# Performance work log

Hardware: AMD Instinct MI355X
Metric: run time of the kernel (lower is better)

The kernel has to match this reference:

```python
import jax, jax.numpy as jnp
import numpy as np

DIM = 256
NUM_HEADS = 4
HEAD_DIM = DIM // NUM_HEADS


def setup_inputs() -> dict:
    key = jax.random.key(0)
    ks = jax.random.split(key, 8)
    B, N, C = 4, 2048, DIM
    x = jax.random.normal(ks[0], (B, N, C), dtype=jnp.float32)
    R = jax.random.normal(ks[1], (B, 3, 3), dtype=jnp.float32)
    P = jax.random.normal(ks[2], (N, 3), dtype=jnp.float32)
    s = 1.0 / np.sqrt(C)
    qkv_w = jax.random.normal(ks[3], (3 * C, C), dtype=jnp.float32) * s
    qkv_b = jax.random.normal(ks[4], (3 * C,), dtype=jnp.float32) * 0.02
    proj_w = jax.random.normal(ks[5], (C, C), dtype=jnp.float32) * s
    proj_b = jax.random.normal(ks[6], (C,), dtype=jnp.float32) * 0.02
    pos_scale = jnp.asarray(1.0, dtype=jnp.float32)
    return {"x": x, "R": R, "P": P, "qkv_w": qkv_w, "qkv_b": qkv_b,
            "proj_w": proj_w, "proj_b": proj_b, "pos_scale": pos_scale}


def reference(x, R, P, qkv_w, qkv_b, proj_w, proj_b, pos_scale):
    B, N, C = x.shape
    H, D = NUM_HEADS, HEAD_DIM
    scale = D ** -0.5
    # qkv: (B,N,3C) -> (3,B,H,N,D)
    qkv = (x @ qkv_w.T + qkv_b).reshape(B, N, 3, H, D).transpose(2, 0, 3, 1, 4)
    q, k, v = qkv[0], qkv[1], qkv[2]
    # attention logits (B,H,N,N)
    attn = jnp.einsum('bhid,bhjd->bhij', q, k) * scale
    # positional bias: RP = (R @ P^T)^T -> (B,N,3); bias_ij = dot(RP_i, P_j)
    RP = jnp.einsum('bab,jb->bja', R, P) if False else jnp.einsum('bca,ja->bjc', jnp.swapaxes(R, 1, 2), P)
    RP = jnp.einsum('bcd,jd->bjc', R, P)  # (B,N,3): (R @ P.T).T
    bias = jnp.einsum('bik,jk->bij', RP, P)[:, None, :, :] * pos_scale  # (B,1,N,N) broadcast over heads
    attn = jax.nn.softmax(attn + bias, axis=-1)
    out = jnp.einsum('bhij,bhjd->bhid', attn, v)  # (B,H,N,D)
    out = out.transpose(0, 2, 1, 3).reshape(B, N, C)
    out = out @ proj_w.T + proj_b
    return out
```

## Files before the change

kernel.cpp:

```cpp
#include <hip/hip_runtime.h>
#include <hip/hip_bf16.h>

#define B_ 4
#define N_ 2048
#define C_ 256
#define H_ 4
#define D_ 64

typedef __attribute__((ext_vector_type(8))) short bf16x8;
typedef __attribute__((ext_vector_type(4))) float f32x4;

#define LOG2E 1.4426950408889634f

static __device__ inline unsigned short f2bf(float f) {
    unsigned u = __builtin_bit_cast(unsigned, f);
    unsigned r = (u + 0x7fffu + ((u >> 16) & 1u)) >> 16;
    return (unsigned short)r;
}
static __device__ inline float bf2f(unsigned short h) {
    unsigned u = ((unsigned)h) << 16;
    return __builtin_bit_cast(float, u);
}
static __device__ inline unsigned pack2(float a, float b) {
    __hip_bfloat162 h = __float22bfloat162_rn(make_float2(a, b));
    unsigned u;
    __builtin_memcpy(&u, &h, 4);
    return u;
}
static __device__ inline bf16x8 ld_frag(const unsigned short* p) {
    return __builtin_bit_cast(bf16x8, *(const uint4*)p);
}

__global__ __launch_bounds__(256) void cvt_kernel(
    const float* __restrict__ x, const float* __restrict__ qkv_w,
    const float* __restrict__ proj_w,
    unsigned short* __restrict__ xb, unsigned short* __restrict__ wqb,
    unsigned short* __restrict__ wpb)
{
    const int bid = blockIdx.x, tid = threadIdx.x;
    const float* s; unsigned short* d; int i;
    if (bid < 1024)      { s = x;      d = xb;  i = (bid * 256 + tid) * 8; }
    else if (bid < 1120) { s = qkv_w;  d = wqb; i = ((bid - 1024) * 256 + tid) * 8; }
    else                 { s = proj_w; d = wpb; i = ((bid - 1120) * 256 + tid) * 8; }
    float4 a = *(const float4*)(s + i);
    float4 b = *(const float4*)(s + i + 4);
    uint4 u;
    u.x = pack2(a.x, a.y); u.y = pack2(a.z, a.w);
    u.z = pack2(b.x, b.y); u.w = pack2(b.z, b.w);
    *(uint4*)(d + i) = u;
}

__global__ __launch_bounds__(256) void qkv_gemm(
    const unsigned short* __restrict__ xb, const unsigned short* __restrict__ wb,
    const float* __restrict__ bias, unsigned short* __restrict__ qb,
    unsigned short* __restrict__ kb, unsigned short* __restrict__ vt)
{
    __shared__ __align__(16) unsigned short As[128 * 40];
    __shared__ __align__(16) unsigned short Bs[128 * 40];
    const int m0 = blockIdx.x * 128, o0 = blockIdx.y * 128;
    const int tid = threadIdx.x;
    const int wave = tid >> 6, lane = tid & 63, quad = lane >> 4, l16 = lane & 15;
    const int wy = wave >> 1, wx = wave & 1;

    f32x4 acc[4][4];
    #pragma unroll
    for (int i = 0; i < 4; ++i)
        #pragma unroll
        for (int j = 0; j < 4; ++j) acc[i][j] = (f32x4){0.f, 0.f, 0.f, 0.f};

    const int srow = tid >> 1, soff = (tid & 1) * 16;

    for (int k0 = 0; k0 < 256; k0 += 32) {
        __syncthreads();
        {
            const unsigned short* sa = &xb[(size_t)(m0 + srow) * 256 + k0 + soff];
            const unsigned short* sb = &wb[(size_t)(o0 + srow) * 256 + k0 + soff];
            *(uint4*)&As[srow * 40 + soff + 0] = *(const uint4*)(sa + 0);
            *(uint4*)&As[srow * 40 + soff + 8] = *(const uint4*)(sa + 8);
            *(uint4*)&Bs[srow * 40 + soff + 0] = *(const uint4*)(sb + 0);
            *(uint4*)&Bs[srow * 40 + soff + 8] = *(const uint4*)(sb + 8);
        }
        __syncthreads();
        bf16x8 a[4], b[4];
        #pragma unroll
        for (int mt = 0; mt < 4; ++mt) a[mt] = ld_frag(&As[(wy * 64 + mt * 16 + l16) * 40 + quad * 8]);
        #pragma unroll
        for (int nt = 0; nt < 4; ++nt) b[nt] = ld_frag(&Bs[(wx * 64 + nt * 16 + l16) * 40 + quad * 8]);
        #pragma unroll
        for (int mt = 0; mt < 4; ++mt)
            #pragma unroll
            for (int nt = 0; nt < 4; ++nt)
                acc[mt][nt] = __builtin_amdgcn_mfma_f32_16x16x32_bf16(a[mt], b[nt], acc[mt][nt], 0, 0, 0);
    }

    const int sec = o0 + wx * 64;
    const int three = sec >> 8;
    const int h = (sec >> 6) & 3;
    const int b = m0 >> 11;
    float bv[4];
    #pragma unroll
    for (int nt = 0; nt < 4; ++nt) bv[nt] = bias[sec + nt * 16 + l16];

    if (three == 2) {
        const int n64 = (m0 + wy * 64) & 2047;
        const size_t bh64 = ((size_t)b * H_ + h) * 64;
        #pragma unroll
        for (int nt = 0; nt < 4; ++nt) {
            int d = nt * 16 + l16;
            #pragma unroll
            for (int r = 0; r < 4; ++r) {
                ushort4 v;
                v.x = f2bf(acc[0][nt][r] + bv[nt]);
                v.y = f2bf(acc[1][nt][r] + bv[nt]);
                v.z = f2bf(acc[2][nt][r] + bv[nt]);
                v.w = f2bf(acc[3][nt][r] + bv[nt]);
                *(ushort4*)&vt[(bh64 + d) * N_ + n64 + 16 * quad + 4 * r] = v;
            }
        }
    } else {
        unsigned short* dst = (three == 0) ? qb : kb;
        float sc = (three == 0) ? (0.125f * LOG2E) : 1.0f;
        #pragma unroll
        for (int mt = 0; mt < 4; ++mt)
            #pragma unroll
            for (int r = 0; r < 4; ++r) {
                int n = (m0 + wy * 64 + mt * 16 + quad * 4 + r) & 2047;
                size_t rowbase = (((size_t)b * H_ + h) * N_ + n) * D_;
                #pragma unroll
                for (int nt = 0; nt < 4; ++nt)
                    dst[rowbase + nt * 16 + l16] = f2bf((acc[mt][nt][r] + bv[nt]) * sc);
            }
    }
}

#define LDK 72
#define LDKX 104

__global__ __launch_bounds__(256) void attn_kernel(
    const unsigned short* __restrict__ qb, const unsigned short* __restrict__ kb,
    const unsigned short* __restrict__ vt,
    const float* __restrict__ Rm, const float* __restrict__ Pm,
    const float* __restrict__ ps_ptr,
    unsigned short* __restrict__ Opart, float* __restrict__ ml)
{
    __shared__ __align__(16) unsigned short Ks[64 * LDKX];
    __shared__ __align__(16) unsigned short Vs[64 * LDK];
    __shared__ __align__(16) unsigned short Ps[64 * LDK];

    const int bh = blockIdx.y;
    const int b = bh >> 2;
    const int i0 = blockIdx.x * 64;
    const int split = blockIdx.z;
    const int tid = threadIdx.x;
    const int wave = tid >> 6, lane = tid & 63;
    const int quad = lane >> 4, l16 = lane & 15;
    const float ps = ps_ptr[0];

    const size_t base = (size_t)bh * N_ * D_;
    const unsigned short* qg = qb + base;
    const unsigned short* kg = kb + base;
    const unsigned short* vg = vt + base;

    if (tid < 64) {
        uint4 z = {0u, 0u, 0u, 0u};
        *(uint4*)&Ks[tid * LDKX + 80] = z;
        *(uint4*)&Ks[tid * LDKX + 88] = z;
    }

    const int qrow = i0 + wave * 16 + l16;
    bf16x8 aq[3];
    #pragma unroll
    for (int ks = 0; ks < 2; ++ks)
        aq[ks] = ld_frag(&qg[(size_t)qrow * D_ + ks * 32 + quad * 8]);

    {
        float p0 = Pm[qrow * 3 + 0], p1 = Pm[qrow * 3 + 1], p2 = Pm[qrow * 3 + 2];
        float sc = ps * LOG2E;
        unsigned short ah[3], al[3];
        #pragma unroll
        for (int c = 0; c < 3; ++c) {
            float a = (Rm[b * 9 + c * 3 + 0] * p0 + Rm[b * 9 + c * 3 + 1] * p1
                     + Rm[b * 9 + c * 3 + 2] * p2) * sc;
            ah[c] = f2bf(a);
            al[c] = f2bf(a - bf2f(ah[c]));
        }
        bf16x8 e = (bf16x8){0,0,0,0,0,0,0,0};
        if (quad == 0) {
            e[0] = (short)ah[0]; e[1] = (short)ah[1]; e[2] = (short)ah[2];
            e[3] = (short)ah[0]; e[4] = (short)ah[1]; e[5] = (short)ah[2];
            e[6] = (short)al[0]; e[7] = (short)al[1];
        } else if (quad == 1) {
            e[0] = (short)al[2];
        }
        aq[2] = e;
    }

    const bf16x8 ones = (bf16x8){0x3F80,0x3F80,0x3F80,0x3F80,0x3F80,0x3F80,0x3F80,0x3F80};

    float m_run = -1e30f;
    f32x4 o_acc[4], lacc;
    #pragma unroll
    for (int t = 0; t < 4; ++t) o_acc[t] = (f32x4){0.f, 0.f, 0.f, 0.f};
    lacc = (f32x4){0.f, 0.f, 0.f, 0.f};

    const int jbeg = split * (N_ / 2);
    const int NT = (N_ / 2) / 64;

    for (int jt = 0; jt < NT; ++jt) {
        const int j0 = jbeg + jt * 64;
        __syncthreads();
        #pragma unroll
        for (int rr = 0; rr < 2; ++rr) {
            int c = tid + rr * 256;
            int row = c >> 3, off = (c & 7) * 8;
            *(uint4*)&Ks[row * LDKX + off] = *(const uint4*)&kg[(size_t)(j0 + row) * D_ + off];
            *(uint4*)&Vs[row * LDK + off] = *(const uint4*)&vg[(size_t)row * N_ + j0 + off];
        }
        if (tid < 64) {
            const float* pp = &Pm[(size_t)(j0 + tid) * 3];
            float p0 = pp[0], p1 = pp[1], p2 = pp[2];
            unsigned u0 = f2bf(p0), u1 = f2bf(p1), u2 = f2bf(p2);
            unsigned v0 = f2bf(p0 - bf2f((unsigned short)u0));
            unsigned v1 = f2bf(p1 - bf2f((unsigned short)u1));
            unsigned v2 = f2bf(p2 - bf2f((unsigned short)u2));
            uint4 lo, hi;
            lo.x = u0 | (u1 << 16); lo.y = u2 | (v0 << 16);
            lo.z = v1 | (v2 << 16); lo.w = u0 | (u1 << 16);
            hi.x = u2; hi.y = 0u; hi.z = 0u; hi.w = 0u;
            *(uint4*)&Ks[tid * LDKX + 64] = lo;
            *(uint4*)&Ks[tid * LDKX + 72] = hi;
        }
        __syncthreads();

        f32x4 s[4];
        #pragma unroll
        for (int t = 0; t < 4; ++t) {
            f32x4 c = {0.f, 0.f, 0.f, 0.f};
            #pragma unroll
            for (int ks = 0; ks < 3; ++ks) {
                bf16x8 bk = ld_frag(&Ks[(l16 + 16 * t) * LDKX + ks * 32 + quad * 8]);
                c = __builtin_amdgcn_mfma_f32_16x16x32_bf16(aq[ks], bk, c, 0, 0, 0);
            }
            s[t] = c;
        }

        float mx = m_run;
        #pragma unroll
        for (int t = 0; t < 4; ++t)
            #pragma unroll
            for (int r = 0; r < 4; ++r)
                mx = fmaxf(mx, s[t][r]);
        #pragma unroll
        for (int off = 1; off < 64; off <<= 1)
            mx = fmaxf(mx, __shfl_xor(mx, off));
        const float alpha = exp2f(m_run - mx);
        m_run = mx;

        #pragma unroll
        for (int r = 0; r < 4; ++r) {
            float p0 = exp2f(s[0][r] - mx), p1 = exp2f(s[1][r] - mx);
            float p2 = exp2f(s[2][r] - mx), p3 = exp2f(s[3][r] - mx);
            uint2 w;
            w.x = pack2(p0, p1);
            w.y = pack2(p2, p3);
            *(uint2*)&Ps[(wave * 16 + quad * 4 + r) * LDK + 4 * l16] = w;
        }

        if (alpha < 1.0f) {
            #pragma unroll
            for (int t = 0; t < 4; ++t)
                #pragma unroll
                for (int r = 0; r < 4; ++r)
                    o_acc[t][r] *= alpha;
            #pragma unroll
            for (int r = 0; r < 4; ++r) lacc[r] *= alpha;
        }

        #pragma unroll
        for (int ks = 0; ks < 2; ++ks) {
            bf16x8 ap = ld_frag(&Ps[(wave * 16 + l16) * LDK + ks * 32 + quad * 8]);
            #pragma unroll
            for (int t = 0; t < 4; ++t) {
                bf16x8 bv = ld_frag(&Vs[(l16 + 16 * t) * LDK + ks * 32 + quad * 8]);
                o_acc[t] = __builtin_amdgcn_mfma_f32_16x16x32_bf16(ap, bv, o_acc[t], 0, 0, 0);
            }
            lacc = __builtin_amdgcn_mfma_f32_16x16x32_bf16(ap, ones, lacc, 0, 0, 0);
        }
    }

    const size_t pbase = (size_t)(split * 16 + bh) * N_;
    #pragma unroll
    for (int r = 0; r < 4; ++r) {
        int row = i0 + wave * 16 + quad * 4 + r;
        #pragma unroll
        for (int t = 0; t < 4; ++t)
            Opart[(pbase + row) * D_ + l16 + 16 * t] = f2bf(o_acc[t][r]);
        if (l16 == 0) {
            float2* mlp = (float2*)ml;
            mlp[pbase + row] = make_float2(m_run, lacc[r]);
        }
    }
}

__global__ __launch_bounds__(256) void proj_gemm(
    const unsigned short* __restrict__ Opart, const float* __restrict__ ml,
    const unsigned short* __restrict__ wb, const float* __restrict__ bias,
    float* __restrict__ out)
{
    __shared__ __align__(16) unsigned short As[64 * 40];
    __shared__ __align__(16) unsigned short Bs[64 * 40];
    const int m0 = blockIdx.x * 64, o0 = blockIdx.y * 64;
    const int tid = threadIdx.x;
    const int wave = tid >> 6, lane = tid & 63, quad = lane >> 4, l16 = lane & 15;
    const float2* mlp = (const float2*)ml;

    const int srow = tid >> 2, scb = (tid & 3) * 8;
    const int sm = m0 + srow, sb = sm >> 11, sn = sm & 2047;

    float w1h[4], w2h[4];
    #pragma unroll
    for (int h = 0; h < 4; ++h) {
        size_t r1 = (size_t)(sb * 4 + h) * N_ + sn;
        float2 ml1 = mlp[r1], ml2 = mlp[r1 + 16 * N_];
        float mm = fmaxf(ml1.x, ml2.x);
        float w1 = exp2f(ml1.x - mm), w2 = exp2f(ml2.x - mm);
        float inv = 1.f / (ml1.y * w1 + ml2.y * w2);
        w1h[h] = w1 * inv; w2h[h] = w2 * inv;
    }

    f32x4 acc[4];
    #pragma unroll
    for (int j = 0; j < 4; ++j) acc[j] = (f32x4){0.f, 0.f, 0.f, 0.f};

    for (int k0 = 0; k0 < 256; k0 += 32) {
        const int h = k0 >> 6;
        const int d0 = (k0 & 63) + scb;
        __syncthreads();
        {
            size_t r1 = (size_t)(sb * 4 + h) * N_ + sn;
            union { uint4 u; unsigned short s[8]; } a1, a2;
            a1.u = *(const uint4*)&Opart[r1 * D_ + d0];
            a2.u = *(const uint4*)&Opart[(r1 + 16 * N_) * D_ + d0];
            float w1 = w1h[h], w2 = w2h[h];
            uint4 mv;
            unsigned* mp = (unsigned*)&mv;
            #pragma unroll
            for (int j = 0; j < 4; ++j)
                mp[j] = pack2(bf2f(a1.s[2*j]) * w1 + bf2f(a2.s[2*j]) * w2,
                              bf2f(a1.s[2*j+1]) * w1 + bf2f(a2.s[2*j+1]) * w2);
            *(uint4*)&As[srow * 40 + scb] = mv;
            *(uint4*)&Bs[srow * 40 + scb] = *(const uint4*)&wb[(size_t)(o0 + srow) * 256 + k0 + scb];
        }
        __syncthreads();
        bf16x8 a = ld_frag(&As[(wave * 16 + l16) * 40 + quad * 8]);
        #pragma unroll
        for (int nt = 0; nt < 4; ++nt) {
            bf16x8 b = ld_frag(&Bs[(nt * 16 + l16) * 40 + quad * 8]);
            acc[nt] = __builtin_amdgcn_mfma_f32_16x16x32_bf16(a, b, acc[nt], 0, 0, 0);
        }
    }

    float bv[4];
    #pragma unroll
    for (int nt = 0; nt < 4; ++nt) bv[nt] = bias[o0 + nt * 16 + l16];
    #pragma unroll
    for (int r = 0; r < 4; ++r) {
        int m = m0 + wave * 16 + quad * 4 + r;
        #pragma unroll
        for (int nt = 0; nt < 4; ++nt)
            out[(size_t)m * 256 + o0 + nt * 16 + l16] = acc[nt][r] + bv[nt];
    }
}

extern "C" void kernel_launch(void* const* d_in, const int* in_sizes, int n_in,
                              void* d_out, int out_size, void* d_ws, size_t ws_size,
                              hipStream_t stream) {
    const float* x       = (const float*)d_in[0];
    const float* Rm      = (const float*)d_in[1];
    const float* Pm      = (const float*)d_in[2];
    const float* qkv_w   = (const float*)d_in[3];
    const float* qkv_b   = (const float*)d_in[4];
    const float* proj_w  = (const float*)d_in[5];
    const float* proj_b  = (const float*)d_in[6];
    const float* pos_scl = (const float*)d_in[7];
    float* out = (float*)d_out;

    const size_t NE = (size_t)B_ * H_ * N_ * D_;
    unsigned short* xb    = (unsigned short*)d_ws;
    unsigned short* wqb   = xb   + NE;
    unsigned short* wpb   = wqb  + 768 * 256;
    unsigned short* qb    = wpb  + 256 * 256;
    unsigned short* kb    = qb   + NE;
    unsigned short* vtb   = kb   + NE;
    unsigned short* opart = vtb  + NE;
    float*          mlb   = (float*)(opart + 2 * NE);

    cvt_kernel<<<1152, 256, 0, stream>>>(x, qkv_w, proj_w, xb, wqb, wpb);
    qkv_gemm<<<dim3(64, 6), 256, 0, stream>>>(xb, wqb, qkv_b, qb, kb, vtb);
    attn_kernel<<<dim3(32, 16, 2), 256, 0, stream>>>(qb, kb, vtb, Rm, Pm, pos_scl, opart, mlb);
    proj_gemm<<<dim3(128, 4), 256, 0, stream>>>(opart, mlb, wpb, proj_b, out);
}
```

Baseline: 140.1 us.

## Replace online softmax max with a precomputed Cauchy-Schwarz upper bound

Computes a per-row upper bound on the logits from the query norm times the max key norm plus the positional-vector norm times the max |P| norm, using a new norm_kernel and a reduction appended to cvt_kernel. The attention loop then exponentiates against this fixed bound instead of tracking a running max. This removes the per-tile max reduction, shuffles and rescaling of the accumulators, and lets the split-combine in the projection reduce to a plain sum. The cost is an extra small kernel and atomics, plus a risk of underflow when the bound is far above the true max, which can lose precision or make the row sum zero.

```diff
diff --git a/kernel.cpp b/kernel.cpp
--- a/kernel.cpp
+++ b/kernel.cpp
@@ -33,10 +33,11 @@
 
 __global__ __launch_bounds__(256) void cvt_kernel(
     const float* __restrict__ x, const float* __restrict__ qkv_w,
-    const float* __restrict__ proj_w,
+    const float* __restrict__ proj_w, const float* __restrict__ Pm,
     unsigned short* __restrict__ xb, unsigned short* __restrict__ wqb,
-    unsigned short* __restrict__ wpb)
+    unsigned short* __restrict__ wpb, unsigned* __restrict__ nb)
 {
+    __shared__ float red[256];
     const int bid = blockIdx.x, tid = threadIdx.x;
     const float* s; unsigned short* d; int i;
     if (bid < 1024)      { s = x;      d = xb;  i = (bid * 256 + tid) * 8; }
@@ -48,6 +49,24 @@
     u.x = pack2(a.x, a.y); u.y = pack2(a.z, a.w);
     u.z = pack2(b.x, b.y); u.w = pack2(b.z, b.w);
     *(uint4*)(d + i) = u;
+
+    if (bid == 1151) {
+        float mp = 0.f;
+        #pragma unroll
+        for (int r = 0; r < 8; ++r) {
+            int n = tid * 8 + r;
+            float p0 = Pm[n * 3 + 0], p1 = Pm[n * 3 + 1], p2 = Pm[n * 3 + 2];
+            mp = fmaxf(mp, p0 * p0 + p1 * p1 + p2 * p2);
+        }
+        red[tid] = mp;
+        __syncthreads();
+        for (int w = 128; w > 0; w >>= 1) {
+            if (tid < w) red[tid] = fmaxf(red[tid], red[tid + w]);
+            __syncthreads();
+        }
+        if (tid < 16) nb[tid] = 0u;
+        if (tid == 0) nb[16] = __builtin_bit_cast(unsigned, red[0]);
+    }
 }
 
 __global__ __launch_bounds__(256) void qkv_gemm(
@@ -133,6 +152,29 @@
     }
 }
 
+__global__ __launch_bounds__(256) void norm_kernel(
+    const unsigned short* __restrict__ kb, unsigned* __restrict__ nb)
+{
+    __shared__ float red[256];
+    const int bh = blockIdx.x, chunk = blockIdx.y, tid = threadIdx.x;
+    const size_t base = (size_t)bh * N_ * D_ + (size_t)(chunk * 256 + tid) * D_;
+    float sk = 0.f;
+    #pragma unroll
+    for (int j4 = 0; j4 < 8; ++j4) {
+        union { uint4 u; unsigned short s[8]; } kv;
+        kv.u = *(const uint4*)&kb[base + j4 * 8];
+        #pragma unroll
+        for (int j = 0; j < 8; ++j) { float v = bf2f(kv.s[j]); sk += v * v; }
+    }
+    red[tid] = sk;
+    __syncthreads();
+    for (int w = 128; w > 0; w >>= 1) {
+        if (tid < w) red[tid] = fmaxf(red[tid], red[tid + w]);
+        __syncthreads();
+    }
+    if (tid == 0) atomicMax(&nb[bh], __builtin_bit_cast(unsigned, red[0]));
+}
+
 #define LDK 72
 #define LDKX 104
 
@@ -140,7 +182,7 @@
     const unsigned short* __restrict__ qb, const unsigned short* __restrict__ kb,
     const unsigned short* __restrict__ vt,
     const float* __restrict__ Rm, const float* __restrict__ Pm,
-    const float* __restrict__ ps_ptr,
+    const float* __restrict__ ps_ptr, const unsigned* __restrict__ nb,
     unsigned short* __restrict__ Opart, float* __restrict__ ml)
 {
     __shared__ __align__(16) unsigned short Ks[64 * LDKX];
@@ -173,17 +215,21 @@
     for (int ks = 0; ks < 2; ++ks)
         aq[ks] = ld_frag(&qg[(size_t)qrow * D_ + ks * 32 + quad * 8]);
 
+    float rpn;
     {
         float p0 = Pm[qrow * 3 + 0], p1 = Pm[qrow * 3 + 1], p2 = Pm[qrow * 3 + 2];
         float sc = ps * LOG2E;
         unsigned short ah[3], al[3];
+        float s2 = 0.f;
         #pragma unroll
         for (int c = 0; c < 3; ++c) {
             float a = (Rm[b * 9 + c * 3 + 0] * p0 + Rm[b * 9 + c * 3 + 1] * p1
                      + Rm[b * 9 + c * 3 + 2] * p2) * sc;
+            s2 += a * a;
             ah[c] = f2bf(a);
             al[c] = f2bf(a - bf2f(ah[c]));
         }
+        rpn = s2;
         bf16x8 e = (bf16x8){0,0,0,0,0,0,0,0};
         if (quad == 0) {
             e[0] = (short)ah[0]; e[1] = (short)ah[1]; e[2] = (short)ah[2];
@@ -195,9 +241,30 @@
         aq[2] = e;
     }
 
+    float Mrow[4];
+    {
+        float qn = 0.f;
+        #pragma unroll
+        for (int ks = 0; ks < 2; ++ks)
+            #pragma unroll
+            for (int j = 0; j < 8; ++j) {
+                float v = bf2f((unsigned short)aq[ks][j]);
+                qn += v * v;
+            }
+        qn += __shfl_xor(qn, 16);
+        qn += __shfl_xor(qn, 32);
+        const float maxK = sqrtf(__builtin_bit_cast(float, nb[bh]));
+        const float maxP = sqrtf(__builtin_bit_cast(float, nb[16]));
+        #pragma unroll
+        for (int r = 0; r < 4; ++r) {
+            float qrn = sqrtf(__shfl(qn, quad * 4 + r));
+            float arn = sqrtf(__shfl(rpn, quad * 4 + r));
+            Mrow[r] = qrn * maxK + arn * maxP + 1.0f;
+        }
+    }
+
     const bf16x8 ones = (bf16x8){0x3F80,0x3F80,0x3F80,0x3F80,0x3F80,0x3F80,0x3F80,0x3F80};
 
-    float m_run = -1e30f;
     f32x4 o_acc[4], lacc;
     #pragma unroll
     for (int t = 0; t < 4; ++t) o_acc[t] = (f32x4){0.f, 0.f, 0.f, 0.f};
@@ -244,36 +311,14 @@
             s[t] = c;
         }
 
-        float mx = m_run;
-        #pragma unroll
-        for (int t = 0; t < 4; ++t)
-            #pragma unroll
-            for (int r = 0; r < 4; ++r)
-                mx = fmaxf(mx, s[t][r]);
-        #pragma unroll
-        for (int off = 1; off < 64; off <<= 1)
-            mx = fmaxf(mx, __shfl_xor(mx, off));
-        const float alpha = exp2f(m_run - mx);
-        m_run = mx;
-
         #pragma unroll
         for (int r = 0; r < 4; ++r) {
-            float p0 = exp2f(s[0][r] - mx), p1 = exp2f(s[1][r] - mx);
-            float p2 = exp2f(s[2][r] - mx), p3 = exp2f(s[3][r] - mx);
+            float p0 = exp2f(s[0][r] - Mrow[r]), p1 = exp2f(s[1][r] - Mrow[r]);
+            float p2 = exp2f(s[2][r] - Mrow[r]), p3 = exp2f(s[3][r] - Mrow[r]);
             uint2 w;
             w.x = pack2(p0, p1);
             w.y = pack2(p2, p3);
             *(uint2*)&Ps[(wave * 16 + quad * 4 + r) * LDK + 4 * l16] = w;
-        }
-
-        if (alpha < 1.0f) {
-            #pragma unroll
-            for (int t = 0; t < 4; ++t)
-                #pragma unroll
-                for (int r = 0; r < 4; ++r)
-                    o_acc[t][r] *= alpha;
-            #pragma unroll
-            for (int r = 0; r < 4; ++r) lacc[r] *= alpha;
         }
 
         #pragma unroll
@@ -295,10 +340,8 @@
         #pragma unroll
         for (int t = 0; t < 4; ++t)
             Opart[(pbase + row) * D_ + l16 + 16 * t] = f2bf(o_acc[t][r]);
-        if (l16 == 0) {
-            float2* mlp = (float2*)ml;
-            mlp[pbase + row] = make_float2(m_run, lacc[r]);
-        }
+        if (l16 == 0)
+            ml[pbase + row] = lacc[r];
     }
 }
 
@@ -312,20 +355,15 @@
     const int m0 = blockIdx.x * 64, o0 = blockIdx.y * 64;
     const int tid = threadIdx.x;
     const int wave = tid >> 6, lane = tid & 63, quad = lane >> 4, l16 = lane & 15;
-    const float2* mlp = (const float2*)ml;
 
     const int srow = tid >> 2, scb = (tid & 3) * 8;
     const int sm = m0 + srow, sb = sm >> 11, sn = sm & 2047;
 
-    float w1h[4], w2h[4];
+    float invh[4];
     #pragma unroll
     for (int h = 0; h < 4; ++h) {
         size_t r1 = (size_t)(sb * 4 + h) * N_ + sn;
-        float2 ml1 = mlp[r1], ml2 = mlp[r1 + 16 * N_];
-        float mm = fmaxf(ml1.x, ml2.x);
-        float w1 = exp2f(ml1.x - mm), w2 = exp2f(ml2.x - mm);
-        float inv = 1.f / (ml1.y * w1 + ml2.y * w2);
-        w1h[h] = w1 * inv; w2h[h] = w2 * inv;
+        invh[h] = 1.f / (ml[r1] + ml[r1 + 16 * (size_t)N_]);
     }
 
     f32x4 acc[4];
@@ -340,14 +378,14 @@
             size_t r1 = (size_t)(sb * 4 + h) * N_ + sn;
             union { uint4 u; unsigned short s[8]; } a1, a2;
             a1.u = *(const uint4*)&Opart[r1 * D_ + d0];
-            a2.u = *(const uint4*)&Opart[(r1 + 16 * N_) * D_ + d0];
-            float w1 = w1h[h], w2 = w2h[h];
+            a2.u = *(const uint4*)&Opart[(r1 + 16 * (size_t)N_) * D_ + d0];
+            float w = invh[h];
             uint4 mv;
             unsigned* mp = (unsigned*)&mv;
             #pragma unroll
             for (int j = 0; j < 4; ++j)
-                mp[j] = pack2(bf2f(a1.s[2*j]) * w1 + bf2f(a2.s[2*j]) * w2,
-                              bf2f(a1.s[2*j+1]) * w1 + bf2f(a2.s[2*j+1]) * w2);
+                mp[j] = pack2((bf2f(a1.s[2*j]) + bf2f(a2.s[2*j])) * w,
+                              (bf2f(a1.s[2*j+1]) + bf2f(a2.s[2*j+1])) * w);
             *(uint4*)&As[srow * 40 + scb] = mv;
             *(uint4*)&Bs[srow * 40 + scb] = *(const uint4*)&wb[(size_t)(o0 + srow) * 256 + k0 + scb];
         }
@@ -394,9 +432,11 @@
     unsigned short* vtb   = kb   + NE;
     unsigned short* opart = vtb  + NE;
     float*          mlb   = (float*)(opart + 2 * NE);
-
-    cvt_kernel<<<1152, 256, 0, stream>>>(x, qkv_w, proj_w, xb, wqb, wpb);
+    unsigned*       nb    = (unsigned*)(mlb + 2 * 16 * 2048);
+
+    cvt_kernel<<<1152, 256, 0, stream>>>(x, qkv_w, proj_w, Pm, xb, wqb, wpb, nb);
     qkv_gemm<<<dim3(64, 6), 256, 0, stream>>>(xb, wqb, qkv_b, qb, kb, vtb);
-    attn_kernel<<<dim3(32, 16, 2), 256, 0, stream>>>(qb, kb, vtb, Rm, Pm, pos_scl, opart, mlb);
+    norm_kernel<<<dim3(16, 8), 256, 0, stream>>>(kb, nb);
+    attn_kernel<<<dim3(32, 16, 2), 256, 0, stream>>>(qb, kb, vtb, Rm, Pm, pos_scl, nb, opart, mlb);
     proj_gemm<<<dim3(128, 4), 256, 0, stream>>>(opart, mlb, wpb, proj_b, out);
 }
```

Result: slower. 147.3 us (+5.2%).
